# Kernel optimization log

Measured on AMD Instinct MI355X. Metric: run time of the kernel, lower is better.

## Reference

```python
import jax, jax.numpy as jnp
import numpy as np

N = 100000   # vertices
M = 20000    # hyperedges
NNZ = 1000000  # incidence pairs
L = 50000    # candidate links
K = 2        # vertices per link
IN, H, OUT = 256, 256, 128


def setup_inputs() -> dict:
    key = jax.random.key(0)
    ks = jax.random.split(key, 8)
    X = jax.random.normal(ks[0], (N, IN), jnp.float32)
    v_idx = jax.random.randint(ks[1], (NNZ,), 0, N, jnp.int32)
    e_idx = jax.random.randint(ks[2], (NNZ,), 0, M, jnp.int32)
    link = jax.random.randint(ks[3], (L, K), 0, N, jnp.int32)
    init = lambda k, sh, fan: jax.random.normal(k, sh, jnp.float32) / np.float32(np.sqrt(fan))
    W1 = init(ks[4], (IN, H), IN)
    b1 = jnp.zeros((H,), jnp.float32)
    W2 = init(ks[5], (H, OUT), H)
    b2 = jnp.zeros((OUT,), jnp.float32)
    fc_w = init(ks[6], (OUT, 1), OUT)
    fc_b = jnp.zeros((1,), jnp.float32)
    return dict(X=X, W1=W1, b1=b1, W2=W2, b2=b2, fc_w=fc_w, fc_b=fc_b,
                v_idx=v_idx, e_idx=e_idx, link=link)


def _segment_mean(vals, idx, num_segments):
    # mean aggregation: segment sum / segment count (count clamped to 1)
    s = jax.ops.segment_sum(vals, idx, num_segments=num_segments)
    c = jax.ops.segment_sum(jnp.ones((idx.shape[0], 1), vals.dtype), idx,
                            num_segments=num_segments)
    return s / jnp.maximum(c, 1.0)


def _hgnn_conv(X, W, b, v_idx, e_idx):
    # theta -> v2e mean -> e2v mean -> ReLU (dropout = identity in eval)
    Xt = X @ W + b                              # [N, d_out]
    Y = _segment_mean(Xt[v_idx], e_idx, M)      # [M, d_out] hyperedge feats
    Xv = _segment_mean(Y[e_idx], v_idx, N)      # [N, d_out] back to vertices
    return jax.nn.relu(Xv)


def reference(X, W1, b1, W2, b2, fc_w, fc_b, v_idx, e_idx, link):
    h1 = _hgnn_conv(X, W1, b1, v_idx, e_idx)    # extra .relu() in encode is idempotent
    h2 = _hgnn_conv(h1, W2, b2, v_idx, e_idx)   # [N, OUT]
    # per-link mean of member vertex embeddings (vectorized gather-mean)
    ex = h2[link].mean(axis=1)                  # [L, OUT]
    return jax.nn.sigmoid(ex @ fc_w + fc_b)     # [L, 1]
```

## Files before the change

kernel.cpp:

```cpp
#include <hip/hip_runtime.h>
#include <cstdint>
#include <cstddef>

#define IN_DIM  256
#define H_DIM   256
#define OUT_DIM 128
#define MEDGES  20000

#define B_E 256
#define B_V 128
#define QN  25600
#define QW  (QN / 2)
#define CT  1024
#define SCAN_T 256

typedef unsigned short u16;
typedef unsigned int   u32;
typedef short bf16x8 __attribute__((ext_vector_type(8)));
typedef float f32x4  __attribute__((ext_vector_type(4)));

__device__ __forceinline__ float bf2f(u16 u) {
    u32 x = ((u32)u) << 16;
    float f;
    __builtin_memcpy(&f, &x, 4);
    return f;
}
__device__ __forceinline__ u16 f2bf(float f) {
    u32 x;
    __builtin_memcpy(&x, &f, 4);
    u32 r = x + 0x7fffu + ((x >> 16) & 1u);
    return (u16)(r >> 16);
}

__global__ void cvt_all(const float4* __restrict__ X,  ushort4* __restrict__ Xb,  int nX,
                        const float4* __restrict__ W1, ushort4* __restrict__ W1b, int nW1,
                        const float4* __restrict__ W2, ushort4* __restrict__ W2b, int nW2)
{
    int i = blockIdx.x * blockDim.x + threadIdx.x;
    const float4* s; ushort4* d; int k;
    if (i < nX)                  { s = X;  d = Xb;  k = i; }
    else if (i < nX + nW1)       { s = W1; d = W1b; k = i - nX; }
    else if (i < nX + nW1 + nW2) { s = W2; d = W2b; k = i - nX - nW1; }
    else return;
    float4 v = s[k];
    ushort4 o;
    o.x = f2bf(v.x); o.y = f2bf(v.y); o.z = f2bf(v.z); o.w = f2bf(v.w);
    d[k] = o;
}

__global__ __launch_bounds__(1024) void count_lds(const int* __restrict__ e_idx,
                                                  const int* __restrict__ v_idx,
                                                  u16* __restrict__ counts_e,
                                                  u16* __restrict__ counts_v,
                                                  int nnz, int m, int n)
{
    __shared__ u32 hist[QW];
    int t = threadIdx.x;
    if ((int)blockIdx.x < B_E) {
        int r = blockIdx.x;
        int chunk = (nnz + B_E - 1) / B_E;
        int beg = r * chunk, end = min(nnz, beg + chunk);
        int ew = (m + 1) >> 1;
        for (int w = t; w < ew; w += CT) hist[w] = 0;
        __syncthreads();
        for (int i = beg + t; i < end; i += CT) {
            int e = e_idx[i];
            atomicAdd(&hist[e >> 1], 1u << ((e & 1) * 16));
        }
        __syncthreads();
        u16* row = counts_e + (size_t)r * m;
        for (int b = t; b < m; b += CT)
            row[b] = (u16)(hist[b >> 1] >> ((b & 1) * 16));
    } else {
        int r = blockIdx.x - B_E;
        int chunk = (nnz + B_V - 1) / B_V;
        int beg = r * chunk, end = min(nnz, beg + chunk);
        u16* row = counts_v + (size_t)r * n;
        for (int q = 0; q < 4; ++q) {
            int qb = q * QN;
            for (int w = t; w < QW; w += CT) hist[w] = 0;
            __syncthreads();
            for (int i = beg + t; i < end; i += CT) {
                unsigned d = (unsigned)(v_idx[i] - qb);
                if (d < (unsigned)QN)
                    atomicAdd(&hist[d >> 1], 1u << ((d & 1) * 16));
            }
            __syncthreads();
            for (int l = t; l < QN && qb + l < n; l += CT)
                row[qb + l] = (u16)(hist[l >> 1] >> ((l & 1) * 16));
            __syncthreads();
        }
    }
}

__global__ __launch_bounds__(SCAN_T) void scan_block_both(u32* __restrict__ counts_e32,
                                                          u32* __restrict__ counts_v32,
                                                          int* __restrict__ e_off,
                                                          int* __restrict__ v_off,
                                                          int* __restrict__ bsums,
                                                          int m, int n, int nbE)
{
    __shared__ int s[SCAN_T];
    u32* mat; int rows; int* out; int* bs; int nwords; int blk;
    if ((int)blockIdx.x < nbE) { mat = counts_e32; rows = B_E; out = e_off; bs = bsums;      nwords = m >> 1; blk = blockIdx.x; }
    else                       { mat = counts_v32; rows = B_V; out = v_off; bs = bsums + 64; nwords = n >> 1; blk = blockIdx.x - nbE; }
    int w = blk * SCAN_T + threadIdx.x;
    u32 a0 = 0, a1 = 0;
    if (w < nwords) {
        for (int r = 0; r < rows; r += 8) {
            u32 v[8];
#pragma unroll
            for (int k = 0; k < 8; ++k) v[k] = mat[(size_t)(r + k) * nwords + w];
#pragma unroll
            for (int k = 0; k < 8; ++k) {
                mat[(size_t)(r + k) * nwords + w] = (a0 & 0xffffu) | (a1 << 16);
                a0 += v[k] & 0xffffu;
                a1 += v[k] >> 16;
            }
        }
    }
    int x = (int)(a0 + a1);
    s[threadIdx.x] = x;
    __syncthreads();
    for (int off = 1; off < SCAN_T; off <<= 1) {
        int v = (threadIdx.x >= off) ? s[threadIdx.x - off] : 0;
        __syncthreads();
        s[threadIdx.x] += v;
        __syncthreads();
    }
    if (w < nwords) {
        int ex = s[threadIdx.x] - x;
        out[2 * w]     = ex;
        out[2 * w + 1] = ex + (int)a0;
    }
    if (threadIdx.x == SCAN_T - 1) bs[blk] = s[SCAN_T - 1];
}

__global__ void scan_top_both(int* __restrict__ bsums, int nbE, int nbV,
                              int* __restrict__ e_off, int* __restrict__ v_off,
                              int m, int n, int nnz)
{
    int t = threadIdx.x;
    if (t == 0) {
        int run = 0;
        for (int i = 0; i < nbE; ++i) { int v = bsums[i]; bsums[i] = run; run += v; }
        e_off[m] = nnz;
    } else if (t == 1) {
        int run = 0;
        for (int i = 0; i < nbV; ++i) { int v = bsums[64 + i]; bsums[64 + i] = run; run += v; }
        v_off[n] = nnz;
    }
}

__global__ void scan_add_both(int* __restrict__ e_off, int* __restrict__ v_off,
                              const int* __restrict__ bsums, int m, int n, int nbE)
{
    int* out; const int* bs; int nwords; int blk;
    if ((int)blockIdx.x < nbE) { out = e_off; bs = bsums;      nwords = m >> 1; blk = blockIdx.x; }
    else                       { out = v_off; bs = bsums + 64; nwords = n >> 1; blk = blockIdx.x - nbE; }
    int w = blk * SCAN_T + threadIdx.x;
    if (w < nwords) {
        int add = bs[blk];
        out[2 * w]     += add;
        out[2 * w + 1] += add;
    }
}

__global__ __launch_bounds__(1024) void scatter_lds(const int* __restrict__ e_idx,
                                                    const int* __restrict__ v_idx,
                                                    const u16* __restrict__ counts_e,
                                                    const u16* __restrict__ counts_v,
                                                    const int* __restrict__ e_off,
                                                    const int* __restrict__ v_off,
                                                    int* __restrict__ e_list,
                                                    int* __restrict__ v_list,
                                                    int nnz, int m, int n)
{
    __shared__ u32 cur[QW];
    int t = threadIdx.x;
    if ((int)blockIdx.x < B_E) {
        int r = blockIdx.x;
        int chunk = (nnz + B_E - 1) / B_E;
        int beg = r * chunk, end = min(nnz, beg + chunk);
        const u32* base = (const u32*)(counts_e + (size_t)r * m);
        int ew = (m + 1) >> 1;
        for (int w = t; w < ew; w += CT) cur[w] = base[w];
        __syncthreads();
        for (int i = beg + t; i < end; i += CT) {
            int e = e_idx[i];
            int sh = (e & 1) * 16;
            u32 old = atomicAdd(&cur[e >> 1], 1u << sh);
            int rel = (int)((old >> sh) & 0xffffu);
            e_list[e_off[e] + rel] = v_idx[i];
        }
    } else {
        int r = blockIdx.x - B_E;
        int chunk = (nnz + B_V - 1) / B_V;
        int beg = r * chunk, end = min(nnz, beg + chunk);
        const u16* row = counts_v + (size_t)r * n;
        for (int q = 0; q < 4; ++q) {
            int qb = q * QN;
            const u32* base = (const u32*)(row + qb);
            int nw = min(QW, (n - qb + 1) >> 1);
            for (int w = t; w < nw; w += CT) cur[w] = base[w];
            __syncthreads();
            for (int i = beg + t; i < end; i += CT) {
                int v = v_idx[i];
                unsigned d = (unsigned)(v - qb);
                if (d < (unsigned)QN) {
                    int sh = (d & 1) * 16;
                    u32 old = atomicAdd(&cur[d >> 1], 1u << sh);
                    int rel = (int)((old >> sh) & 0xffffu);
                    v_list[v_off[v] + rel] = e_idx[i];
                }
            }
            __syncthreads();
        }
    }
}

__global__ void seg_mean_w4(const ushort4* __restrict__ src, ushort4* __restrict__ dst,
                            const int* __restrict__ off, const int* __restrict__ lst,
                            int nseg, int do_relu)
{
    int wid  = (blockIdx.x * blockDim.x + threadIdx.x) >> 6;
    int lane = threadIdx.x & 63;
    if (wid >= nseg) return;
    int beg = __builtin_amdgcn_readfirstlane(off[wid]);
    int end = __builtin_amdgcn_readfirstlane(off[wid + 1]);
    float ax = 0.f, ay = 0.f, az = 0.f, aw = 0.f;
    int j = beg;
    for (; j + 3 < end; j += 4) {
        int i0 = lst[j], i1 = lst[j + 1], i2 = lst[j + 2], i3 = lst[j + 3];
        ushort4 a = src[(size_t)i0 * 64 + lane];
        ushort4 b = src[(size_t)i1 * 64 + lane];
        ushort4 c = src[(size_t)i2 * 64 + lane];
        ushort4 d = src[(size_t)i3 * 64 + lane];
        ax += bf2f(a.x) + bf2f(b.x) + bf2f(c.x) + bf2f(d.x);
        ay += bf2f(a.y) + bf2f(b.y) + bf2f(c.y) + bf2f(d.y);
        az += bf2f(a.z) + bf2f(b.z) + bf2f(c.z) + bf2f(d.z);
        aw += bf2f(a.w) + bf2f(b.w) + bf2f(c.w) + bf2f(d.w);
    }
    for (; j < end; ++j) {
        ushort4 a = src[(size_t)lst[j] * 64 + lane];
        ax += bf2f(a.x); ay += bf2f(a.y); az += bf2f(a.z); aw += bf2f(a.w);
    }
    int cnt = end - beg;
    float inv = (cnt > 0) ? 1.f / (float)cnt : 0.f;
    ax *= inv; ay *= inv; az *= inv; aw *= inv;
    if (do_relu) {
        ax = fmaxf(ax, 0.f); ay = fmaxf(ay, 0.f);
        az = fmaxf(az, 0.f); aw = fmaxf(aw, 0.f);
    }
    ushort4 o;
    o.x = f2bf(ax); o.y = f2bf(ay); o.z = f2bf(az); o.w = f2bf(aw);
    dst[(size_t)wid * 64 + lane] = o;
}

__global__ void seg_mean_w2(const ushort2* __restrict__ src, ushort2* __restrict__ dst,
                            const int* __restrict__ off, const int* __restrict__ lst,
                            int nseg, int do_relu)
{
    int wid  = (blockIdx.x * blockDim.x + threadIdx.x) >> 6;
    int lane = threadIdx.x & 63;
    if (wid >= nseg) return;
    int beg = __builtin_amdgcn_readfirstlane(off[wid]);
    int end = __builtin_amdgcn_readfirstlane(off[wid + 1]);
    float ax = 0.f, ay = 0.f;
    int j = beg;
    for (; j + 3 < end; j += 4) {
        int i0 = lst[j], i1 = lst[j + 1], i2 = lst[j + 2], i3 = lst[j + 3];
        ushort2 a = src[(size_t)i0 * 64 + lane];
        ushort2 b = src[(size_t)i1 * 64 + lane];
        ushort2 c = src[(size_t)i2 * 64 + lane];
        ushort2 d = src[(size_t)i3 * 64 + lane];
        ax += bf2f(a.x) + bf2f(b.x) + bf2f(c.x) + bf2f(d.x);
        ay += bf2f(a.y) + bf2f(b.y) + bf2f(c.y) + bf2f(d.y);
    }
    for (; j < end; ++j) {
        ushort2 a = src[(size_t)lst[j] * 64 + lane];
        ax += bf2f(a.x); ay += bf2f(a.y);
    }
    int cnt = end - beg;
    float inv = (cnt > 0) ? 1.f / (float)cnt : 0.f;
    ax *= inv; ay *= inv;
    if (do_relu) { ax = fmaxf(ax, 0.f); ay = fmaxf(ay, 0.f); }
    ushort2 o;
    o.x = f2bf(ax); o.y = f2bf(ay);
    dst[(size_t)wid * 64 + lane] = o;
}

#define GSTRIDE 40
__global__ __launch_bounds__(256) void gemm_mfma_bf16(const u16* __restrict__ A,
                                                      const u16* __restrict__ W,
                                                      const float* __restrict__ bias,
                                                      u16* __restrict__ C,
                                                      int R, int K, int Cc)
{
    __shared__ __align__(16) u16 As[64 * GSTRIDE];
    __shared__ __align__(16) u16 Bs[64 * GSTRIDE];

    int tid  = threadIdx.x;
    int wave = tid >> 6;
    int lane = tid & 63;
    int quad = lane >> 4;
    int l16  = lane & 15;

    int row0 = blockIdx.y * 64;
    int col0 = blockIdx.x * 64;

    f32x4 acc[4] = {};

    int ar   = tid >> 2;
    int aseg = tid & 3;
    int bk   = tid >> 3;
    int bn   = tid & 7;

    for (int k0 = 0; k0 < K; k0 += 32) {
        bf16x8 av = {};
        int gr = row0 + ar;
        if (gr < R) av = *(const bf16x8*)&A[(size_t)gr * K + k0 + 8 * aseg];
        *(bf16x8*)&As[ar * GSTRIDE + 8 * aseg] = av;
        bf16x8 wv = *(const bf16x8*)&W[(size_t)(k0 + bk) * Cc + col0 + 8 * bn];
#pragma unroll
        for (int j = 0; j < 8; ++j)
            Bs[(8 * bn + j) * GSTRIDE + bk] = ((const u16*)&wv)[j];
        __syncthreads();

        bf16x8 af = *(const bf16x8*)&As[(16 * wave + l16) * GSTRIDE + 8 * quad];
#pragma unroll
        for (int nt = 0; nt < 4; ++nt) {
            bf16x8 bfv = *(const bf16x8*)&Bs[(16 * nt + l16) * GSTRIDE + 8 * quad];
            acc[nt] = __builtin_amdgcn_mfma_f32_16x16x32_bf16(af, bfv, acc[nt], 0, 0, 0);
        }
        __syncthreads();
    }

#pragma unroll
    for (int nt = 0; nt < 4; ++nt) {
        int col = col0 + 16 * nt + l16;
        float bv = bias[col];
#pragma unroll
        for (int r = 0; r < 4; ++r) {
            int grow = row0 + 16 * wave + 4 * quad + r;
            if (grow < R) C[(size_t)grow * Cc + col] = f2bf(acc[nt][r] + bv);
        }
    }
}

__global__ void link_head(const ushort2* __restrict__ h2, const int* __restrict__ link,
                          const float* __restrict__ fc_w, const float* __restrict__ fc_b,
                          float* __restrict__ out, int L)
{
    int gtid = blockIdx.x * blockDim.x + threadIdx.x;
    int wid  = gtid >> 6;
    int lane = threadIdx.x & 63;
    if (wid >= L) return;
    const int Dh = OUT_DIM / 2;
    int a = link[2 * wid + 0];
    int b = link[2 * wid + 1];
    ushort2 ra = h2[(size_t)a * Dh + lane];
    ushort2 rb = h2[(size_t)b * Dh + lane];
    float2 w = *(const float2*)&fc_w[2 * lane];
    float acc = 0.5f * ((bf2f(ra.x) + bf2f(rb.x)) * w.x + (bf2f(ra.y) + bf2f(rb.y)) * w.y);
#pragma unroll
    for (int off = 32; off; off >>= 1) acc += __shfl_xor(acc, off, 64);
    if (lane == 0) out[wid] = 1.f / (1.f + expf(-(acc + fc_b[0])));
}


static inline size_t align_up(size_t x, size_t a) { return (x + a - 1) & ~(a - 1); }

extern "C" void kernel_launch(void* const* d_in, const int* in_sizes, int n_in,
                              void* d_out, int out_size, void* d_ws, size_t ws_size,
                              hipStream_t stream)
{
    const float* X   = (const float*)d_in[0];
    const float* W1  = (const float*)d_in[1];
    const float* b1  = (const float*)d_in[2];
    const float* W2  = (const float*)d_in[3];
    const float* b2  = (const float*)d_in[4];
    const float* fcw = (const float*)d_in[5];
    const float* fcb = (const float*)d_in[6];
    const int* v_idx = (const int*)d_in[7];
    const int* e_idx = (const int*)d_in[8];
    const int* link  = (const int*)d_in[9];
    float* out = (float*)d_out;

    const int NNZ = in_sizes[7];
    const int N   = in_sizes[0] / IN_DIM;
    const int L   = in_sizes[9] / 2;
    const int M   = MEDGES;

    char* p = (char*)d_ws;
    auto carve = [&](size_t bytes) -> void* {
        void* r = (void*)p;
        p += align_up(bytes, 256);
        return r;
    };
    u16*  Xb    = (u16*)carve((size_t)N * IN_DIM * 2);
    u16*  h1b   = (u16*)carve((size_t)N * H_DIM * 2);
    u16*  Aggb  = (u16*)carve((size_t)M * H_DIM * 2);
    u16*  Yb    = (u16*)carve((size_t)M * H_DIM * 2);
    u16*  W1b   = (u16*)carve((size_t)IN_DIM * H_DIM * 2);
    u16*  W2b   = (u16*)carve((size_t)H_DIM * OUT_DIM * 2);
    int*  e_off = (int*)carve((size_t)(M + 1) * 4);
    int*  v_off = (int*)carve((size_t)(N + 1) * 4);
    int*  e_lst = (int*)carve((size_t)NNZ * 4);
    int*  v_lst = (int*)carve((size_t)NNZ * 4);
    int*  bsums = (int*)carve(2048);

    u16* counts_e = (u16*)h1b;
    u16* counts_v = (u16*)((char*)h1b + (size_t)B_E * M * 2);

    const int tb = 256;

    int nX  = N * IN_DIM / 4;
    int nW1 = IN_DIM * H_DIM / 4;
    int nW2 = H_DIM * OUT_DIM / 4;
    cvt_all<<<(nX + nW1 + nW2 + tb - 1) / tb, tb, 0, stream>>>(
        (const float4*)X, (ushort4*)Xb, nX,
        (const float4*)W1, (ushort4*)W1b, nW1,
        (const float4*)W2, (ushort4*)W2b, nW2);

    count_lds<<<B_E + B_V, CT, 0, stream>>>(e_idx, v_idx, counts_e, counts_v, NNZ, M, N);

    int nbE = (M / 2 + SCAN_T - 1) / SCAN_T;
    int nbV = (N / 2 + SCAN_T - 1) / SCAN_T;
    scan_block_both<<<nbE + nbV, SCAN_T, 0, stream>>>((u32*)counts_e, (u32*)counts_v,
                                                      e_off, v_off, bsums, M, N, nbE);
    scan_top_both<<<1, 64, 0, stream>>>(bsums, nbE, nbV, e_off, v_off, M, N, NNZ);
    scan_add_both<<<nbE + nbV, SCAN_T, 0, stream>>>(e_off, v_off, bsums, M, N, nbE);

    scatter_lds<<<B_E + B_V, CT, 0, stream>>>(e_idx, v_idx, counts_e, counts_v,
                                              e_off, v_off, e_lst, v_lst, NNZ, M, N);

    seg_mean_w4<<<((size_t)M * 64 + tb - 1) / tb, tb, 0, stream>>>(
        (const ushort4*)Xb, (ushort4*)Aggb, e_off, e_lst, M, 0);
    gemm_mfma_bf16<<<dim3(H_DIM / 64, (M + 63) / 64), 256, 0, stream>>>(Aggb, W1b, b1, Yb, M, IN_DIM, H_DIM);
    seg_mean_w4<<<((size_t)N * 64 + tb - 1) / tb, tb, 0, stream>>>(
        (const ushort4*)Yb, (ushort4*)h1b, v_off, v_lst, N, 1);

    seg_mean_w4<<<((size_t)M * 64 + tb - 1) / tb, tb, 0, stream>>>(
        (const ushort4*)h1b, (ushort4*)Aggb, e_off, e_lst, M, 0);
    gemm_mfma_bf16<<<dim3(OUT_DIM / 64, (M + 63) / 64), 256, 0, stream>>>(Aggb, W2b, b2, Yb, M, H_DIM, OUT_DIM);
    seg_mean_w2<<<((size_t)N * 64 + tb - 1) / tb, tb, 0, stream>>>(
        (const ushort2*)Yb, (ushort2*)Xb, v_off, v_lst, N, 1);

    link_head<<<((size_t)L * 64 + tb - 1) / tb, tb, 0, stream>>>(
        (const ushort2*)Xb, link, fcw, fcb, out, L);
}
```

Baseline: 557.4 us.

## Pack CSR build counters into bytes with fewer partitions; unroll gather by eight

The counting-sort CSR build now packs four 8-bit counters per word and uses 64 partition rows per side instead of 256/128, so the vertex histogram covers the range in two LDS passes instead of four. This shrinks the count matrices scanned and rewritten by the prefix-scan kernels, and lets offsets be written as int4. The segment-mean kernels also issue eight independent gathers per iteration to raise memory-level parallelism. The risk is that 8-bit counts overflow if any segment's total degree reaches 256, and fewer blocks lowers parallelism in the count and scatter kernels.

Result: faster. 520.3 us (-6.7%).

```diff
diff --git a/kernel.cpp b/kernel.cpp
--- a/kernel.cpp
+++ b/kernel.cpp
@@ -7,10 +7,11 @@
 #define OUT_DIM 128
 #define MEDGES  20000
 
-#define B_E 256
-#define B_V 128
-#define QN  25600
-#define QW  (QN / 2)
+#define B_E 64
+#define B_V 64
+#define ROWS 64
+#define QN2 51200
+#define QW2 (QN2 / 4)
 #define CT  1024
 #define SCAN_T 256
 
@@ -50,44 +51,45 @@
 
 __global__ __launch_bounds__(1024) void count_lds(const int* __restrict__ e_idx,
                                                   const int* __restrict__ v_idx,
-                                                  u16* __restrict__ counts_e,
-                                                  u16* __restrict__ counts_v,
+                                                  u32* __restrict__ counts_e32,
+                                                  u32* __restrict__ counts_v32,
                                                   int nnz, int m, int n)
 {
-    __shared__ u32 hist[QW];
+    __shared__ u32 hist[QW2];
     int t = threadIdx.x;
     if ((int)blockIdx.x < B_E) {
         int r = blockIdx.x;
         int chunk = (nnz + B_E - 1) / B_E;
         int beg = r * chunk, end = min(nnz, beg + chunk);
-        int ew = (m + 1) >> 1;
+        int ew = (m + 3) >> 2;
         for (int w = t; w < ew; w += CT) hist[w] = 0;
         __syncthreads();
         for (int i = beg + t; i < end; i += CT) {
             int e = e_idx[i];
-            atomicAdd(&hist[e >> 1], 1u << ((e & 1) * 16));
-        }
-        __syncthreads();
-        u16* row = counts_e + (size_t)r * m;
-        for (int b = t; b < m; b += CT)
-            row[b] = (u16)(hist[b >> 1] >> ((b & 1) * 16));
+            atomicAdd(&hist[e >> 2], 1u << ((e & 3) * 8));
+        }
+        __syncthreads();
+        u32* row = counts_e32 + (size_t)r * ew;
+        for (int w = t; w < ew; w += CT) row[w] = hist[w];
     } else {
         int r = blockIdx.x - B_E;
         int chunk = (nnz + B_V - 1) / B_V;
         int beg = r * chunk, end = min(nnz, beg + chunk);
-        u16* row = counts_v + (size_t)r * n;
-        for (int q = 0; q < 4; ++q) {
-            int qb = q * QN;
-            for (int w = t; w < QW; w += CT) hist[w] = 0;
+        int vw = (n + 3) >> 2;
+        u32* row = counts_v32 + (size_t)r * vw;
+        for (int q = 0; q < 2; ++q) {
+            int w0 = q * QW2;
+            int nw = min(QW2, vw - w0);
+            int b0 = w0 * 4;
+            for (int w = t; w < QW2; w += CT) hist[w] = 0;
             __syncthreads();
             for (int i = beg + t; i < end; i += CT) {
-                unsigned d = (unsigned)(v_idx[i] - qb);
-                if (d < (unsigned)QN)
-                    atomicAdd(&hist[d >> 1], 1u << ((d & 1) * 16));
+                unsigned d = (unsigned)(v_idx[i] - b0);
+                if (d < (unsigned)(4 * nw))
+                    atomicAdd(&hist[d >> 2], 1u << ((d & 3) * 8));
             }
             __syncthreads();
-            for (int l = t; l < QN && qb + l < n; l += CT)
-                row[qb + l] = (u16)(hist[l >> 1] >> ((l & 1) * 16));
+            for (int w = t; w < nw; w += CT) row[w0 + w] = hist[w];
             __syncthreads();
         }
     }
@@ -101,25 +103,25 @@
                                                           int m, int n, int nbE)
 {
     __shared__ int s[SCAN_T];
-    u32* mat; int rows; int* out; int* bs; int nwords; int blk;
-    if ((int)blockIdx.x < nbE) { mat = counts_e32; rows = B_E; out = e_off; bs = bsums;      nwords = m >> 1; blk = blockIdx.x; }
-    else                       { mat = counts_v32; rows = B_V; out = v_off; bs = bsums + 64; nwords = n >> 1; blk = blockIdx.x - nbE; }
+    u32* mat; int* out; int* bs; int nwords; int blk; int nn;
+    if ((int)blockIdx.x < nbE) { mat = counts_e32; out = e_off; bs = bsums;      nwords = (m + 3) >> 2; blk = blockIdx.x;       nn = m; }
+    else                       { mat = counts_v32; out = v_off; bs = bsums + 64; nwords = (n + 3) >> 2; blk = blockIdx.x - nbE; nn = n; }
     int w = blk * SCAN_T + threadIdx.x;
-    u32 a0 = 0, a1 = 0;
+    u32 a = 0;
     if (w < nwords) {
-        for (int r = 0; r < rows; r += 8) {
+        for (int r = 0; r < ROWS; r += 8) {
             u32 v[8];
 #pragma unroll
             for (int k = 0; k < 8; ++k) v[k] = mat[(size_t)(r + k) * nwords + w];
 #pragma unroll
             for (int k = 0; k < 8; ++k) {
-                mat[(size_t)(r + k) * nwords + w] = (a0 & 0xffffu) | (a1 << 16);
-                a0 += v[k] & 0xffffu;
-                a1 += v[k] >> 16;
+                mat[(size_t)(r + k) * nwords + w] = a;
+                a += v[k];
             }
         }
     }
-    int x = (int)(a0 + a1);
+    int b0 = a & 0xff, b1 = (a >> 8) & 0xff, b2 = (a >> 16) & 0xff, b3 = (int)(a >> 24);
+    int x = b0 + b1 + b2 + b3;
     s[threadIdx.x] = x;
     __syncthreads();
     for (int off = 1; off < SCAN_T; off <<= 1) {
@@ -130,8 +132,16 @@
     }
     if (w < nwords) {
         int ex = s[threadIdx.x] - x;
-        out[2 * w]     = ex;
-        out[2 * w + 1] = ex + (int)a0;
+        int base = 4 * w;
+        if (base + 3 < nn) {
+            int4 o; o.x = ex; o.y = ex + b0; o.z = ex + b0 + b1; o.w = ex + b0 + b1 + b2;
+            *(int4*)&out[base] = o;
+        } else {
+            if (base     < nn) out[base]     = ex;
+            if (base + 1 < nn) out[base + 1] = ex + b0;
+            if (base + 2 < nn) out[base + 2] = ex + b0 + b1;
+            if (base + 3 < nn) out[base + 3] = ex + b0 + b1 + b2;
+        }
     }
     if (threadIdx.x == SCAN_T - 1) bs[blk] = s[SCAN_T - 1];
 }
@@ -155,62 +165,72 @@
 __global__ void scan_add_both(int* __restrict__ e_off, int* __restrict__ v_off,
                               const int* __restrict__ bsums, int m, int n, int nbE)
 {
-    int* out; const int* bs; int nwords; int blk;
-    if ((int)blockIdx.x < nbE) { out = e_off; bs = bsums;      nwords = m >> 1; blk = blockIdx.x; }
-    else                       { out = v_off; bs = bsums + 64; nwords = n >> 1; blk = blockIdx.x - nbE; }
+    int* out; const int* bs; int nwords; int blk; int nn;
+    if ((int)blockIdx.x < nbE) { out = e_off; bs = bsums;      nwords = (m + 3) >> 2; blk = blockIdx.x;       nn = m; }
+    else                       { out = v_off; bs = bsums + 64; nwords = (n + 3) >> 2; blk = blockIdx.x - nbE; nn = n; }
     int w = blk * SCAN_T + threadIdx.x;
     if (w < nwords) {
         int add = bs[blk];
-        out[2 * w]     += add;
-        out[2 * w + 1] += add;
+        int base = 4 * w;
+        if (base + 3 < nn) {
+            int4 o = *(int4*)&out[base];
+            o.x += add; o.y += add; o.z += add; o.w += add;
+            *(int4*)&out[base] = o;
+        } else {
+            if (base     < nn) out[base]     += add;
+            if (base + 1 < nn) out[base + 1] += add;
+            if (base + 2 < nn) out[base + 2] += add;
+            if (base + 3 < nn) out[base + 3] += add;
+        }
     }
 }
 
 __global__ __launch_bounds__(1024) void scatter_lds(const int* __restrict__ e_idx,
                                                     const int* __restrict__ v_idx,
-                                                    const u16* __restrict__ counts_e,
-                                                    const u16* __restrict__ counts_v,
+                                                    const u32* __restrict__ counts_e32,
+                                                    const u32* __restrict__ counts_v32,
                                                     const int* __restrict__ e_off,
                                                     const int* __restrict__ v_off,
                                                     int* __restrict__ e_list,
                                                     int* __restrict__ v_list,
                                                     int nnz, int m, int n)
 {
-    __shared__ u32 cur[QW];
+    __shared__ u32 cur[QW2];
     int t = threadIdx.x;
     if ((int)blockIdx.x < B_E) {
         int r = blockIdx.x;
         int chunk = (nnz + B_E - 1) / B_E;
         int beg = r * chunk, end = min(nnz, beg + chunk);
-        const u32* base = (const u32*)(counts_e + (size_t)r * m);
-        int ew = (m + 1) >> 1;
+        int ew = (m + 3) >> 2;
+        const u32* base = counts_e32 + (size_t)r * ew;
         for (int w = t; w < ew; w += CT) cur[w] = base[w];
         __syncthreads();
         for (int i = beg + t; i < end; i += CT) {
             int e = e_idx[i];
-            int sh = (e & 1) * 16;
-            u32 old = atomicAdd(&cur[e >> 1], 1u << sh);
-            int rel = (int)((old >> sh) & 0xffffu);
+            int sh = (e & 3) * 8;
+            u32 old = atomicAdd(&cur[e >> 2], 1u << sh);
+            int rel = (int)((old >> sh) & 0xffu);
             e_list[e_off[e] + rel] = v_idx[i];
         }
     } else {
         int r = blockIdx.x - B_E;
         int chunk = (nnz + B_V - 1) / B_V;
         int beg = r * chunk, end = min(nnz, beg + chunk);
-        const u16* row = counts_v + (size_t)r * n;
-        for (int q = 0; q < 4; ++q) {
-            int qb = q * QN;
-            const u32* base = (const u32*)(row + qb);
-            int nw = min(QW, (n - qb + 1) >> 1);
-            for (int w = t; w < nw; w += CT) cur[w] = base[w];
+        int vw = (n + 3) >> 2;
+        const u32* row = counts_v32 + (size_t)r * vw;
+        for (int q = 0; q < 2; ++q) {
+            int w0 = q * QW2;
+            int nw = min(QW2, vw - w0);
+            int b0 = w0 * 4;
+            for (int w = t; w < nw; w += CT) cur[w] = row[w0 + w];
             __syncthreads();
             for (int i = beg + t; i < end; i += CT) {
                 int v = v_idx[i];
-                unsigned d = (unsigned)(v - qb);
-                if (d < (unsigned)QN) {
-                    int sh = (d & 1) * 16;
-                    u32 old = atomicAdd(&cur[d >> 1], 1u << sh);
-                    int rel = (int)((old >> sh) & 0xffffu);
+                unsigned d = (unsigned)(v - b0);
+                if (d < (unsigned)(4 * nw)) {
+                    int sh = (d & 3) * 8;
+                    u32 old = atomicAdd(&cur[d >> 2], 1u << sh);
+                    int rel = (int)((old >> sh) & 0xffu);
                     v_list[v_off[v] + rel] = e_idx[i];
                 }
             }
@@ -230,16 +250,25 @@
     int end = __builtin_amdgcn_readfirstlane(off[wid + 1]);
     float ax = 0.f, ay = 0.f, az = 0.f, aw = 0.f;
     int j = beg;
+    for (; j + 7 < end; j += 8) {
+        ushort4 r[8];
+#pragma unroll
+        for (int k = 0; k < 8; ++k) r[k] = src[(size_t)lst[j + k] * 64 + lane];
+#pragma unroll
+        for (int k = 0; k < 8; ++k) {
+            ax += bf2f(r[k].x); ay += bf2f(r[k].y);
+            az += bf2f(r[k].z); aw += bf2f(r[k].w);
+        }
+    }
     for (; j + 3 < end; j += 4) {
-        int i0 = lst[j], i1 = lst[j + 1], i2 = lst[j + 2], i3 = lst[j + 3];
-        ushort4 a = src[(size_t)i0 * 64 + lane];
-        ushort4 b = src[(size_t)i1 * 64 + lane];
-        ushort4 c = src[(size_t)i2 * 64 + lane];
-        ushort4 d = src[(size_t)i3 * 64 + lane];
-        ax += bf2f(a.x) + bf2f(b.x) + bf2f(c.x) + bf2f(d.x);
-        ay += bf2f(a.y) + bf2f(b.y) + bf2f(c.y) + bf2f(d.y);
-        az += bf2f(a.z) + bf2f(b.z) + bf2f(c.z) + bf2f(d.z);
-        aw += bf2f(a.w) + bf2f(b.w) + bf2f(c.w) + bf2f(d.w);
+        ushort4 r[4];
+#pragma unroll
+        for (int k = 0; k < 4; ++k) r[k] = src[(size_t)lst[j + k] * 64 + lane];
+#pragma unroll
+        for (int k = 0; k < 4; ++k) {
+            ax += bf2f(r[k].x); ay += bf2f(r[k].y);
+            az += bf2f(r[k].z); aw += bf2f(r[k].w);
+        }
     }
     for (; j < end; ++j) {
         ushort4 a = src[(size_t)lst[j] * 64 + lane];
@@ -268,14 +297,19 @@
     int end = __builtin_amdgcn_readfirstlane(off[wid + 1]);
     float ax = 0.f, ay = 0.f;
     int j = beg;
+    for (; j + 7 < end; j += 8) {
+        ushort2 r[8];
+#pragma unroll
+        for (int k = 0; k < 8; ++k) r[k] = src[(size_t)lst[j + k] * 64 + lane];
+#pragma unroll
+        for (int k = 0; k < 8; ++k) { ax += bf2f(r[k].x); ay += bf2f(r[k].y); }
+    }
     for (; j + 3 < end; j += 4) {
-        int i0 = lst[j], i1 = lst[j + 1], i2 = lst[j + 2], i3 = lst[j + 3];
-        ushort2 a = src[(size_t)i0 * 64 + lane];
-        ushort2 b = src[(size_t)i1 * 64 + lane];
-        ushort2 c = src[(size_t)i2 * 64 + lane];
-        ushort2 d = src[(size_t)i3 * 64 + lane];
-        ax += bf2f(a.x) + bf2f(b.x) + bf2f(c.x) + bf2f(d.x);
-        ay += bf2f(a.y) + bf2f(b.y) + bf2f(c.y) + bf2f(d.y);
+        ushort2 r[4];
+#pragma unroll
+        for (int k = 0; k < 4; ++k) r[k] = src[(size_t)lst[j + k] * 64 + lane];
+#pragma unroll
+        for (int k = 0; k < 4; ++k) { ax += bf2f(r[k].x); ay += bf2f(r[k].y); }
     }
     for (; j < end; ++j) {
         ushort2 a = src[(size_t)lst[j] * 64 + lane];
@@ -410,8 +444,9 @@
     int*  v_lst = (int*)carve((size_t)NNZ * 4);
     int*  bsums = (int*)carve(2048);
 
-    u16* counts_e = (u16*)h1b;
-    u16* counts_v = (u16*)((char*)h1b + (size_t)B_E * M * 2);
+    int EW = (M + 3) >> 2;
+    u32* counts_e32 = (u32*)h1b;
+    u32* counts_v32 = counts_e32 + (size_t)B_E * EW;
 
     const int tb = 256;
 
@@ -423,16 +458,16 @@
         (const float4*)W1, (ushort4*)W1b, nW1,
         (const float4*)W2, (ushort4*)W2b, nW2);
 
-    count_lds<<<B_E + B_V, CT, 0, stream>>>(e_idx, v_idx, counts_e, counts_v, NNZ, M, N);
-
-    int nbE = (M / 2 + SCAN_T - 1) / SCAN_T;
-    int nbV = (N / 2 + SCAN_T - 1) / SCAN_T;
-    scan_block_both<<<nbE + nbV, SCAN_T, 0, stream>>>((u32*)counts_e, (u32*)counts_v,
+    count_lds<<<B_E + B_V, CT, 0, stream>>>(e_idx, v_idx, counts_e32, counts_v32, NNZ, M, N);
+
+    int nbE = (((M + 3) >> 2) + SCAN_T - 1) / SCAN_T;
+    int nbV = (((N + 3) >> 2) + SCAN_T - 1) / SCAN_T;
+    scan_block_both<<<nbE + nbV, SCAN_T, 0, stream>>>(counts_e32, counts_v32,
                                                       e_off, v_off, bsums, M, N, nbE);
     scan_top_both<<<1, 64, 0, stream>>>(bsums, nbE, nbV, e_off, v_off, M, N, NNZ);
     scan_add_both<<<nbE + nbV, SCAN_T, 0, stream>>>(e_off, v_off, bsums, M, N, nbE);
 
-    scatter_lds<<<B_E + B_V, CT, 0, stream>>>(e_idx, v_idx, counts_e, counts_v,
+    scatter_lds<<<B_E + B_V, CT, 0, stream>>>(e_idx, v_idx, counts_e32, counts_v32,
                                               e_off, v_off, e_lst, v_lst, NNZ, M, N);
 
     seg_mean_w4<<<((size_t)M * 64 + tb - 1) / tb, tb, 0, stream>>>(
```
